# Optimization experiments

Hardware: AMD Instinct MI355X
Metric: run time of the kernel (lower is better)

## Reference

```python
import jax, jax.numpy as jnp
import numpy as np

B, S, D, H = 64, 197, 1024, 4096

# I-BERT IntGELU constants: erf(x) ~ a*(x+b)^2 + c on [0,-b], integer-only form
K_SQRT2 = 1.4142          # sqrt(2)
GELU_SHIFT = 14           # 2**14 right-shift to avoid accumulator overflow
COEF_A = -0.2888
COEF_B = -1.769
COEF_C = 1.0 / COEF_A     # c folded by a, as in I-BERT (coeff[2] /= coeff[0])


def setup_inputs() -> dict:
    key = jax.random.key(0)
    k1, k2, k3, k4, k5, k6 = jax.random.split(key, 6)
    x_int = jax.random.randint(k1, (B, S, D), 0, 127).astype(jnp.int32)  # int8-range activations
    s_x = jax.random.uniform(k2, (1,), jnp.float32, 0.01, 0.03)          # per-tensor act scale
    w1 = jax.random.normal(k3, (H, D), jnp.float32) * 0.02
    b1 = jax.random.normal(k4, (H,), jnp.float32) * 0.02
    w2 = jax.random.normal(k5, (D, H), jnp.float32) * 0.02
    b2 = jax.random.normal(k6, (D,), jnp.float32) * 0.02
    return {"x_int": x_int, "s_x": s_x, "w1": w1, "b1": b1, "w2": w2, "b2": b2}


def _quant_weight(w):
    # per-tensor symmetric int8 weight quantization (QuantLinearWithWeight)
    s_w = jnp.max(jnp.abs(w)) / 127.0
    w_int = jnp.clip(jnp.round(w / s_w), -127.0, 127.0)
    return w_int, s_w


def _quant_linear(x_int, s_x, w, b):
    # integer GEMM: int8 acts x int8 weights -> int32 accumulator, scale s_x*s_w
    w_int, s_w = _quant_weight(w)
    s_out = s_x * s_w
    b_int = jnp.round(b / s_out)  # bias quantized into the accumulator scale
    acc = jnp.einsum('bsd,hd->bsh', x_int, w_int) + b_int
    return acc, s_out


def _int_erf(x_int, sf):
    # integer polynomial approx of erf (I-BERT)
    b_int = jnp.floor(COEF_B / sf)
    c_int = jnp.floor(COEF_C / sf ** 2)
    sign = jnp.sign(x_int)
    abs_int = jnp.minimum(jnp.abs(x_int), -b_int)
    y_int = sign * ((abs_int + b_int) ** 2 + c_int)
    sf_out = sf ** 2 * COEF_A
    y_int = jnp.floor(y_int / 2.0 ** GELU_SHIFT)  # shift to keep accumulator in range
    return y_int, sf_out * 2.0 ** GELU_SHIFT


def _int_gelu(x_int, sf):
    # GELU(x) = x * 0.5 * (1 + erf(x/sqrt(2))), integer-only
    sig_int, sig_sf = _int_erf(x_int, sf / K_SQRT2)
    shift_int = jnp.floor(1.0 / sig_sf)  # torch: 1.0 // sigmoid_scaling_factor
    y_int = x_int * (sig_int + shift_int)
    return y_int, sf * sig_sf / 2.0


def _quant_act(x_int, sf):
    # QuantAct: requantize int32-scale activations back to int8 (dynamic per-tensor scale)
    x_hat = x_int * sf
    s_a = jnp.max(jnp.abs(x_hat)) / 127.0
    q = jnp.clip(jnp.round(x_hat / s_a), -128.0, 127.0)
    return q, s_a


def reference(x_int, s_x, w1, b1, w2, b2):
    x = x_int.astype(jnp.float32)
    s = s_x[0]
    x, s = _quant_linear(x, s, w1, b1)   # [B,S,H] int32 accumulator
    x, s = _int_gelu(x, s)               # integer-only GELU
    x, s = _quant_act(x, s)              # requant -> int8 range
    # dropout_1 is identity in eval mode
    x, s = _quant_linear(x, s, w2, b2)   # [B,S,D] int32 accumulator
    # dropout_2 is identity in eval mode
    return x, s
```

## Files before the change

kernel.cpp:

```cpp
#include <hip/hip_runtime.h>
#include <cstdint>
#include <cstddef>

constexpr int Bb = 64, Ss = 197, Dd = 1024, Hh = 4096;
constexpr int M  = Bb * Ss;
constexpr int MT = (M + 127) / 128;
constexpr int Mpad = MT * 128;
constexpr int NSLOT = 128;

#define SL_MAXW1 0
#define SL_MAXW2 1
#define SL_S1    4
#define SL_BERF  5
#define SL_CERF  6
#define SL_SHIFT 7
#define SL_S2    8
#define SL_SA    9
#define SL_SOUT2 10
#define SL_SW1   11
#define SL_SW2   12
#define SL_MAXY0 16

typedef int v4i __attribute__((ext_vector_type(4)));

#define GLD_LDS(g, l) \
  __builtin_amdgcn_global_load_lds((const __attribute__((address_space(1))) void*)(g), \
                                   (__attribute__((address_space(3))) void*)(l), 16, 0, 0)

__global__ void k_init(unsigned* sl) {
  int t = threadIdx.x;
  if (t < 16 + NSLOT) sl[t] = 0u;
}

__global__ void k_absmax(const float* __restrict__ src, int n4, unsigned* slot) {
  const float4* s4 = (const float4*)src;
  float m = 0.f;
  for (int i = blockIdx.x * blockDim.x + threadIdx.x; i < n4; i += gridDim.x * blockDim.x) {
    float4 v = s4[i];
    m = fmaxf(m, fmaxf(fmaxf(fabsf(v.x), fabsf(v.y)), fmaxf(fabsf(v.z), fabsf(v.w))));
  }
  #pragma unroll
  for (int off = 32; off; off >>= 1) m = fmaxf(m, __shfl_down(m, off, 64));
  __shared__ float wm[4];
  int lane = threadIdx.x & 63, wid = threadIdx.x >> 6;
  if (lane == 0) wm[wid] = m;
  __syncthreads();
  if (threadIdx.x == 0) {
    float b = wm[0];
    for (int i = 1; i < (int)(blockDim.x >> 6); i++) b = fmaxf(b, wm[i]);
    atomicMax(slot, __float_as_uint(b));
  }
}

__global__ void k_scalars1(unsigned* slu, const float* s_x_ptr) {
  float* slf = (float*)slu;
  float s_w1 = __uint_as_float(slu[SL_MAXW1]) / 127.0f;
  float s_w2 = __uint_as_float(slu[SL_MAXW2]) / 127.0f;
  float s1  = s_x_ptr[0] * s_w1;
  float sfe = s1 / 1.4142f;
  float berf = floorf(-1.769f / sfe);
  float cerf = floorf(((float)(1.0 / -0.2888)) / (sfe * sfe));
  float sig  = ((sfe * sfe) * -0.2888f) * 16384.0f;
  float shiftv = floorf(1.0f / sig);
  float s2 = (s1 * sig) / 2.0f;
  slf[SL_S1] = s1; slf[SL_BERF] = berf; slf[SL_CERF] = cerf;
  slf[SL_SHIFT] = shiftv; slf[SL_S2] = s2; slf[SL_SW1] = s_w1; slf[SL_SW2] = s_w2;
}

__global__ void k_scalars2(unsigned* slu, float* dout_scalar) {
  float* slf = (float*)slu;
  float maxy = 0.f;
  for (int i = 0; i < NSLOT; i++) maxy = fmaxf(maxy, __uint_as_float(slu[SL_MAXY0 + i]));
  float xm = fabsf(maxy * slf[SL_S2]);
  float sa = xm / 127.0f;
  float sout2 = sa * slf[SL_SW2];
  slf[SL_SA] = sa; slf[SL_SOUT2] = sout2;
  *dout_scalar = sout2;
}

__global__ void k_quant_w(const float* __restrict__ w, int8_t* __restrict__ wq, int n4,
                          const unsigned* __restrict__ slu, int swslot) {
  float sw = ((const float*)slu)[swslot];
  const float4* w4 = (const float4*)w;
  for (int i = blockIdx.x * blockDim.x + threadIdx.x; i < n4; i += gridDim.x * blockDim.x) {
    float4 v = w4[i];
    int qa = (int)fminf(fmaxf(rintf(v.x / sw), -127.f), 127.f);
    int qb = (int)fminf(fmaxf(rintf(v.y / sw), -127.f), 127.f);
    int qc = (int)fminf(fmaxf(rintf(v.z / sw), -127.f), 127.f);
    int qd = (int)fminf(fmaxf(rintf(v.w / sw), -127.f), 127.f);
    ((unsigned*)wq)[i] = (unsigned)(qa & 0xff) | ((unsigned)(qb & 0xff) << 8) |
                         ((unsigned)(qc & 0xff) << 16) | ((unsigned)(qd & 0xff) << 24);
  }
}

__global__ void k_cvt_x(const int* __restrict__ x, int8_t* __restrict__ xq, int n4, int npad4) {
  const int4* x4 = (const int4*)x;
  for (int i = blockIdx.x * blockDim.x + threadIdx.x; i < npad4; i += gridDim.x * blockDim.x) {
    unsigned p = 0u;
    if (i < n4) {
      int4 v = x4[i];
      p = (unsigned)(v.x & 0xff) | ((unsigned)(v.y & 0xff) << 8) |
          ((unsigned)(v.z & 0xff) << 16) | ((unsigned)(v.w & 0xff) << 24);
    }
    ((unsigned*)xq)[i] = p;
  }
}

template <int K, int MODE, int GN>
__global__ __launch_bounds__(256) void k_gemm(
    const int8_t* __restrict__ A, const int8_t* __restrict__ Bm,
    const float* __restrict__ bias, const unsigned* __restrict__ slu,
    int8_t* __restrict__ qout, float* __restrict__ fout, unsigned* maxslot,
    int Mreal, int Ncols) {
  __shared__ alignas(16) int8_t smem[32768];
  int8_t* As = smem;
  int8_t* Bs = smem + 16384;
  const int t = threadIdx.x;
  const int id = blockIdx.x;
  const int chunk = gridDim.x >> 3;
  const int newid = (id & 7) * chunk + (id >> 3);
  const int bm = newid / GN, bn = newid % GN;
  const int lane = t & 63, wid = t >> 6;
  const int wRow = (wid >> 1) * 64, wCol = (wid & 1) * 64;
  const int lm = lane & 15, quad = lane >> 4;

  v4i acc[4][4] = {};

  const size_t aBase = (size_t)bm * 128 * K;
  const size_t bBase = (size_t)bn * 128 * K;

  for (int k0 = 0; k0 < K; k0 += 128) {
    #pragma unroll
    for (int c = 0; c < 4; c++) {
      int s = c * 256 + t;
      int row = s >> 3;
      int cb = (s & 7) ^ (row & 7);
      size_t goff = (size_t)row * K + k0 + cb * 16;
      GLD_LDS(A + aBase + goff, As + s * 16);
      GLD_LDS(Bm + bBase + goff, Bs + s * 16);
    }
    __syncthreads();
    #pragma unroll
    for (int ks = 0; ks < 2; ks++) {
      v4i af[4], bf[4];
      #pragma unroll
      for (int i = 0; i < 4; i++) {
        int r = wRow + i * 16 + lm;
        af[i] = *(const v4i*)(As + r * 128 + (((ks * 4 + quad) ^ (r & 7)) << 4));
      }
      #pragma unroll
      for (int i = 0; i < 4; i++) {
        int r = wCol + i * 16 + lm;
        bf[i] = *(const v4i*)(Bs + r * 128 + (((ks * 4 + quad) ^ (r & 7)) << 4));
      }
      #pragma unroll
      for (int i = 0; i < 4; i++)
        #pragma unroll
        for (int j = 0; j < 4; j++)
          acc[i][j] = __builtin_amdgcn_mfma_i32_16x16x64_i8(bf[j], af[i], acc[i][j], 0, 0, 0);
    }
    __syncthreads();
  }

  const float* slf = (const float*)slu;
  if constexpr (MODE == 2) {
    float sout2 = slf[SL_SOUT2];
    float4 bq[4];
    #pragma unroll
    for (int j = 0; j < 4; j++) {
      float4 bv = *(const float4*)(bias + bn * 128 + wCol + j * 16 + quad * 4);
      bq[j].x = rintf(bv.x / sout2); bq[j].y = rintf(bv.y / sout2);
      bq[j].z = rintf(bv.z / sout2); bq[j].w = rintf(bv.w / sout2);
    }
    #pragma unroll
    for (int i = 0; i < 4; i++) {
      int gr = bm * 128 + wRow + i * 16 + lm;
      if (gr < Mreal) {
        #pragma unroll
        for (int j = 0; j < 4; j++) {
          int gc0 = bn * 128 + wCol + j * 16 + quad * 4;
          float4 o;
          o.x = (float)acc[i][j][0] + bq[j].x;
          o.y = (float)acc[i][j][1] + bq[j].y;
          o.z = (float)acc[i][j][2] + bq[j].z;
          o.w = (float)acc[i][j][3] + bq[j].w;
          *(float4*)(fout + (size_t)gr * Ncols + gc0) = o;
        }
      }
    }
  } else {
    float s1 = slf[SL_S1], berf = slf[SL_BERF], cerf = slf[SL_CERF], shiftv = slf[SL_SHIFT];
    float s2 = slf[SL_S2];
    float sa = (MODE == 1) ? slf[SL_SA] : 1.0f;
    float r_req = (MODE == 1) ? (s2 / sa) : 1.0f;
    float lmax = 0.f;
    float4 bq[4];
    #pragma unroll
    for (int j = 0; j < 4; j++) {
      float4 bv = *(const float4*)(bias + bn * 128 + wCol + j * 16 + quad * 4);
      bq[j].x = rintf(bv.x / s1); bq[j].y = rintf(bv.y / s1);
      bq[j].z = rintf(bv.z / s1); bq[j].w = rintf(bv.w / s1);
    }
    #pragma unroll
    for (int i = 0; i < 4; i++) {
      int mrow = wRow + i * 16 + lm;
      int gr = bm * 128 + mrow;
      bool rowok = gr < Mreal;
      #pragma unroll
      for (int j = 0; j < 4; j++) {
        int n0 = wCol + j * 16 + quad * 4;
        unsigned packed = 0u;
        #pragma unroll
        for (int r = 0; r < 4; r++) {
          float a = (float)acc[i][j][r] + ((const float*)&bq[j])[r];
          float sgn = (a > 0.f) ? 1.f : ((a < 0.f) ? -1.f : 0.f);
          float ax = fminf(fabsf(a), -berf);
          float tt = ax + berf;
          float yv = sgn * (tt * tt + cerf);
          yv = floorf(yv * (1.0f / 16384.0f));
          float y = a * (yv + shiftv);
          if constexpr (MODE == 0) {
            if (rowok) lmax = fmaxf(lmax, fabsf(y));
          } else {
            float qf = rintf(y * r_req);
            qf = fminf(fmaxf(qf, -128.f), 127.f);
            packed |= ((unsigned)((int)qf & 0xff)) << (8 * r);
          }
        }
        if constexpr (MODE == 1) {
          *(unsigned*)(smem + mrow * 132 + n0) = packed;
        }
      }
    }
    if constexpr (MODE == 0) {
      #pragma unroll
      for (int off = 32; off; off >>= 1) lmax = fmaxf(lmax, __shfl_down(lmax, off, 64));
      float* red = (float*)smem;
      if (lane == 0) red[wid] = lmax;
      __syncthreads();
      if (t == 0) {
        float b = fmaxf(fmaxf(red[0], red[1]), fmaxf(red[2], red[3]));
        atomicMax(maxslot + (id & (NSLOT - 1)), __float_as_uint(b));
      }
    } else {
      __syncthreads();
      #pragma unroll
      for (int c2 = 0; c2 < 4; c2++) {
        int idx = c2 * 256 + t;
        int row = idx >> 3, c16 = (idx & 7) << 4;
        v4i v = *(const v4i*)(smem + row * 132 + c16);
        *(v4i*)(qout + (size_t)(bm * 128 + row) * Ncols + bn * 128 + c16) = v;
      }
    }
  }
}

extern "C" void kernel_launch(void* const* d_in, const int* in_sizes, int n_in,
                              void* d_out, int out_size, void* d_ws, size_t ws_size,
                              hipStream_t stream) {
  const int*   x   = (const int*)d_in[0];
  const float* s_x = (const float*)d_in[1];
  const float* w1  = (const float*)d_in[2];
  const float* b1  = (const float*)d_in[3];
  const float* w2  = (const float*)d_in[4];
  const float* b2  = (const float*)d_in[5];
  float* out = (float*)d_out;

  char* ws = (char*)d_ws;
  unsigned* slots = (unsigned*)ws;
  int8_t* w1q = (int8_t*)(ws + 1024);
  int8_t* w2q = w1q + (size_t)Hh * Dd;
  int8_t* xq  = w2q + (size_t)Dd * Hh;
  int8_t* qbuf = xq + (size_t)Mpad * Dd;

  k_init<<<1, 256, 0, stream>>>(slots);
  k_absmax<<<512, 256, 0, stream>>>(w1, Hh * Dd / 4, slots + SL_MAXW1);
  k_absmax<<<512, 256, 0, stream>>>(w2, Dd * Hh / 4, slots + SL_MAXW2);
  k_scalars1<<<1, 1, 0, stream>>>(slots, s_x);
  k_quant_w<<<512, 256, 0, stream>>>(w1, w1q, Hh * Dd / 4, slots, SL_SW1);
  k_quant_w<<<512, 256, 0, stream>>>(w2, w2q, Dd * Hh / 4, slots, SL_SW2);
  k_cvt_x<<<512, 256, 0, stream>>>(x, xq, M * Dd / 4, Mpad * Dd / 4);

  const int g1 = (Hh / 128) * MT;
  k_gemm<Dd, 0, Hh / 128><<<g1, 256, 0, stream>>>(xq, w1q, b1, slots, nullptr, nullptr,
                                                  slots + SL_MAXY0, M, Hh);
  k_scalars2<<<1, 1, 0, stream>>>(slots, out + (size_t)M * Dd);
  k_gemm<Dd, 1, Hh / 128><<<g1, 256, 0, stream>>>(xq, w1q, b1, slots, qbuf, nullptr,
                                                  nullptr, M, Hh);
  const int g2 = (Dd / 128) * MT;
  k_gemm<Hh, 2, Dd / 128><<<g2, 256, 0, stream>>>(qbuf, w2q, b2, slots, nullptr, out,
                                                  nullptr, M, Dd);
}
```

Before: 428.5 us.

## Enlarge int8 GEMM block tile to 256x128 with one wave per 64-row strip

The int8 MFMA GEMM block tile grows from 128x128 to 256x128. Each wave now owns a 64x128 strip with a 4x8 accumulator array, so it issues more MFMAs per LDS fragment load. LDS grows to 48KB, the launch becomes a 2D grid, and the XCD-aware block-id swizzle is dropped. The change raises arithmetic intensity per byte loaded. In exchange it adds register pressure, lowers occupancy, leaves fewer blocks to fill the CUs, and makes L2 locality depend on default block ordering.

```diff
diff --git a/kernel.cpp b/kernel.cpp
--- a/kernel.cpp
+++ b/kernel.cpp
@@ -4,8 +4,8 @@
 
 constexpr int Bb = 64, Ss = 197, Dd = 1024, Hh = 4096;
 constexpr int M  = Bb * Ss;
-constexpr int MT = (M + 127) / 128;
-constexpr int Mpad = MT * 128;
+constexpr int MT2 = (M + 255) / 256;
+constexpr int Mpad = MT2 * 256;
 constexpr int NSLOT = 128;
 
 #define SL_MAXW1 0
@@ -106,57 +106,59 @@
   }
 }
 
-template <int K, int MODE, int GN>
+template <int K, int MODE>
 __global__ __launch_bounds__(256) void k_gemm(
     const int8_t* __restrict__ A, const int8_t* __restrict__ Bm,
     const float* __restrict__ bias, const unsigned* __restrict__ slu,
     int8_t* __restrict__ qout, float* __restrict__ fout, unsigned* maxslot,
     int Mreal, int Ncols) {
-  __shared__ alignas(16) int8_t smem[32768];
+  __shared__ alignas(16) int8_t smem[49152];
   int8_t* As = smem;
-  int8_t* Bs = smem + 16384;
+  int8_t* Bs = smem + 32768;
   const int t = threadIdx.x;
-  const int id = blockIdx.x;
-  const int chunk = gridDim.x >> 3;
-  const int newid = (id & 7) * chunk + (id >> 3);
-  const int bm = newid / GN, bn = newid % GN;
+  const int bn = blockIdx.x, bm = blockIdx.y;
   const int lane = t & 63, wid = t >> 6;
-  const int wRow = (wid >> 1) * 64, wCol = (wid & 1) * 64;
+  const int wR = wid * 64;
   const int lm = lane & 15, quad = lane >> 4;
 
-  v4i acc[4][4] = {};
-
-  const size_t aBase = (size_t)bm * 128 * K;
+  v4i acc[4][8] = {};
+
+  const size_t aBase = (size_t)bm * 256 * K;
   const size_t bBase = (size_t)bn * 128 * K;
 
   for (int k0 = 0; k0 < K; k0 += 128) {
+    #pragma unroll
+    for (int c = 0; c < 8; c++) {
+      int s = c * 256 + t;
+      int row = s >> 3;
+      int cb = (s & 7) ^ (row & 7);
+      GLD_LDS(A + aBase + (size_t)row * K + k0 + cb * 16, As + s * 16);
+    }
     #pragma unroll
     for (int c = 0; c < 4; c++) {
       int s = c * 256 + t;
       int row = s >> 3;
       int cb = (s & 7) ^ (row & 7);
-      size_t goff = (size_t)row * K + k0 + cb * 16;
-      GLD_LDS(A + aBase + goff, As + s * 16);
-      GLD_LDS(Bm + bBase + goff, Bs + s * 16);
+      GLD_LDS(Bm + bBase + (size_t)row * K + k0 + cb * 16, Bs + s * 16);
     }
     __syncthreads();
     #pragma unroll
     for (int ks = 0; ks < 2; ks++) {
-      v4i af[4], bf[4];
+      v4i af[4], bf[8];
       #pragma unroll
       for (int i = 0; i < 4; i++) {
-        int r = wRow + i * 16 + lm;
+        int r = wR + i * 16 + lm;
         af[i] = *(const v4i*)(As + r * 128 + (((ks * 4 + quad) ^ (r & 7)) << 4));
       }
       #pragma unroll
-      for (int i = 0; i < 4; i++) {
-        int r = wCol + i * 16 + lm;
-        bf[i] = *(const v4i*)(Bs + r * 128 + (((ks * 4 + quad) ^ (r & 7)) << 4));
+      for (int j = 0; j < 8; j++) {
+        int r = j * 16 + lm;
+        bf[j] = *(const v4i*)(Bs + r * 128 + (((ks * 4 + quad) ^ (r & 7)) << 4));
       }
       #pragma unroll
       for (int i = 0; i < 4; i++)
         #pragma unroll
-        for (int j = 0; j < 4; j++)
+        for (int j = 0; j < 8; j++)
           acc[i][j] = __builtin_amdgcn_mfma_i32_16x16x64_i8(bf[j], af[i], acc[i][j], 0, 0, 0);
     }
     __syncthreads();
@@ -165,20 +167,20 @@
   const float* slf = (const float*)slu;
   if constexpr (MODE == 2) {
     float sout2 = slf[SL_SOUT2];
-    float4 bq[4];
-    #pragma unroll
-    for (int j = 0; j < 4; j++) {
-      float4 bv = *(const float4*)(bias + bn * 128 + wCol + j * 16 + quad * 4);
+    float4 bq[8];
+    #pragma unroll
+    for (int j = 0; j < 8; j++) {
+      float4 bv = *(const float4*)(bias + bn * 128 + j * 16 + quad * 4);
       bq[j].x = rintf(bv.x / sout2); bq[j].y = rintf(bv.y / sout2);
       bq[j].z = rintf(bv.z / sout2); bq[j].w = rintf(bv.w / sout2);
     }
     #pragma unroll
     for (int i = 0; i < 4; i++) {
-      int gr = bm * 128 + wRow + i * 16 + lm;
+      int gr = bm * 256 + wR + i * 16 + lm;
       if (gr < Mreal) {
         #pragma unroll
-        for (int j = 0; j < 4; j++) {
-          int gc0 = bn * 128 + wCol + j * 16 + quad * 4;
+        for (int j = 0; j < 8; j++) {
+          int gc0 = bn * 128 + j * 16 + quad * 4;
           float4 o;
           o.x = (float)acc[i][j][0] + bq[j].x;
           o.y = (float)acc[i][j][1] + bq[j].y;
@@ -194,21 +196,21 @@
     float sa = (MODE == 1) ? slf[SL_SA] : 1.0f;
     float r_req = (MODE == 1) ? (s2 / sa) : 1.0f;
     float lmax = 0.f;
-    float4 bq[4];
-    #pragma unroll
-    for (int j = 0; j < 4; j++) {
-      float4 bv = *(const float4*)(bias + bn * 128 + wCol + j * 16 + quad * 4);
+    float4 bq[8];
+    #pragma unroll
+    for (int j = 0; j < 8; j++) {
+      float4 bv = *(const float4*)(bias + bn * 128 + j * 16 + quad * 4);
       bq[j].x = rintf(bv.x / s1); bq[j].y = rintf(bv.y / s1);
       bq[j].z = rintf(bv.z / s1); bq[j].w = rintf(bv.w / s1);
     }
     #pragma unroll
     for (int i = 0; i < 4; i++) {
-      int mrow = wRow + i * 16 + lm;
-      int gr = bm * 128 + mrow;
+      int mrow = wR + i * 16 + lm;
+      int gr = bm * 256 + mrow;
       bool rowok = gr < Mreal;
       #pragma unroll
-      for (int j = 0; j < 4; j++) {
-        int n0 = wCol + j * 16 + quad * 4;
+      for (int j = 0; j < 8; j++) {
+        int n0 = j * 16 + quad * 4;
         unsigned packed = 0u;
         #pragma unroll
         for (int r = 0; r < 4; r++) {
@@ -240,16 +242,17 @@
       __syncthreads();
       if (t == 0) {
         float b = fmaxf(fmaxf(red[0], red[1]), fmaxf(red[2], red[3]));
+        int id = blockIdx.y * gridDim.x + blockIdx.x;
         atomicMax(maxslot + (id & (NSLOT - 1)), __float_as_uint(b));
       }
     } else {
       __syncthreads();
       #pragma unroll
-      for (int c2 = 0; c2 < 4; c2++) {
+      for (int c2 = 0; c2 < 8; c2++) {
         int idx = c2 * 256 + t;
         int row = idx >> 3, c16 = (idx & 7) << 4;
         v4i v = *(const v4i*)(smem + row * 132 + c16);
-        *(v4i*)(qout + (size_t)(bm * 128 + row) * Ncols + bn * 128 + c16) = v;
+        *(v4i*)(qout + (size_t)(bm * 256 + row) * Ncols + bn * 128 + c16) = v;
       }
     }
   }
@@ -281,13 +284,13 @@
   k_quant_w<<<512, 256, 0, stream>>>(w2, w2q, Dd * Hh / 4, slots, SL_SW2);
   k_cvt_x<<<512, 256, 0, stream>>>(x, xq, M * Dd / 4, Mpad * Dd / 4);
 
-  const int g1 = (Hh / 128) * MT;
-  k_gemm<Dd, 0, Hh / 128><<<g1, 256, 0, stream>>>(xq, w1q, b1, slots, nullptr, nullptr,
-                                                  slots + SL_MAXY0, M, Hh);
+  dim3 g1(Hh / 128, MT2);
+  k_gemm<Dd, 0><<<g1, 256, 0, stream>>>(xq, w1q, b1, slots, nullptr, nullptr,
+                                        slots + SL_MAXY0, M, Hh);
   k_scalars2<<<1, 1, 0, stream>>>(slots, out + (size_t)M * Dd);
-  k_gemm<Dd, 1, Hh / 128><<<g1, 256, 0, stream>>>(xq, w1q, b1, slots, qbuf, nullptr,
-                                                  nullptr, M, Hh);
-  const int g2 = (Dd / 128) * MT;
-  k_gemm<Hh, 2, Dd / 128><<<g2, 256, 0, stream>>>(qbuf, w2q, b2, slots, nullptr, out,
-                                                  nullptr, M, Dd);
-}
+  k_gemm<Dd, 1><<<g1, 256, 0, stream>>>(xq, w1q, b1, slots, qbuf, nullptr,
+                                        nullptr, M, Hh);
+  dim3 g2(Dd / 128, MT2);
+  k_gemm<Hh, 2><<<g2, 256, 0, stream>>>(qbuf, w2q, b2, slots, nullptr, out,
+                                        nullptr, M, Dd);
+}
```

Measured after the change: 583.3 us. 1.36x slower.

## Fuse prologue kernels and replace atomic max slots with per-block partials

Applied to the files above, without the earlier changes.

Merges the two weight absmax kernels into one launch and the weight-quantize and activation-convert kernels into one launch. Drops the init kernel by writing per-block partial maxima to workspace arrays and reducing them in parallel scalar kernels, instead of using atomicMax slots. Replaces the XCD-aware block swizzle in the GEMMs with a plain 2D grid, and simplifies the sign handling in the GELU epilogue. Fewer launches and no atomics, at the risk of losing the L2 locality the swizzle provided.

```diff
diff --git a/kernel.cpp b/kernel.cpp
--- a/kernel.cpp
+++ b/kernel.cpp
@@ -6,10 +6,8 @@
 constexpr int M  = Bb * Ss;
 constexpr int MT = (M + 127) / 128;
 constexpr int Mpad = MT * 128;
-constexpr int NSLOT = 128;
-
-#define SL_MAXW1 0
-#define SL_MAXW2 1
+constexpr int NBLK1 = (Hh / 128) * MT;
+
 #define SL_S1    4
 #define SL_BERF  5
 #define SL_CERF  6
@@ -19,7 +17,6 @@
 #define SL_SOUT2 10
 #define SL_SW1   11
 #define SL_SW2   12
-#define SL_MAXY0 16
 
 typedef int v4i __attribute__((ext_vector_type(4)));
 
@@ -27,99 +24,125 @@
   __builtin_amdgcn_global_load_lds((const __attribute__((address_space(1))) void*)(g), \
                                    (__attribute__((address_space(3))) void*)(l), 16, 0, 0)
 
-__global__ void k_init(unsigned* sl) {
-  int t = threadIdx.x;
-  if (t < 16 + NSLOT) sl[t] = 0u;
-}
-
-__global__ void k_absmax(const float* __restrict__ src, int n4, unsigned* slot) {
-  const float4* s4 = (const float4*)src;
-  float m = 0.f;
-  for (int i = blockIdx.x * blockDim.x + threadIdx.x; i < n4; i += gridDim.x * blockDim.x) {
-    float4 v = s4[i];
-    m = fmaxf(m, fmaxf(fmaxf(fabsf(v.x), fabsf(v.y)), fmaxf(fabsf(v.z), fabsf(v.w))));
-  }
+__device__ __forceinline__ float blockmax256(float m) {
   #pragma unroll
   for (int off = 32; off; off >>= 1) m = fmaxf(m, __shfl_down(m, off, 64));
   __shared__ float wm[4];
   int lane = threadIdx.x & 63, wid = threadIdx.x >> 6;
   if (lane == 0) wm[wid] = m;
   __syncthreads();
-  if (threadIdx.x == 0) {
-    float b = wm[0];
-    for (int i = 1; i < (int)(blockDim.x >> 6); i++) b = fmaxf(b, wm[i]);
-    atomicMax(slot, __float_as_uint(b));
-  }
-}
-
-__global__ void k_scalars1(unsigned* slu, const float* s_x_ptr) {
-  float* slf = (float*)slu;
-  float s_w1 = __uint_as_float(slu[SL_MAXW1]) / 127.0f;
-  float s_w2 = __uint_as_float(slu[SL_MAXW2]) / 127.0f;
-  float s1  = s_x_ptr[0] * s_w1;
-  float sfe = s1 / 1.4142f;
-  float berf = floorf(-1.769f / sfe);
-  float cerf = floorf(((float)(1.0 / -0.2888)) / (sfe * sfe));
-  float sig  = ((sfe * sfe) * -0.2888f) * 16384.0f;
-  float shiftv = floorf(1.0f / sig);
-  float s2 = (s1 * sig) / 2.0f;
-  slf[SL_S1] = s1; slf[SL_BERF] = berf; slf[SL_CERF] = cerf;
-  slf[SL_SHIFT] = shiftv; slf[SL_S2] = s2; slf[SL_SW1] = s_w1; slf[SL_SW2] = s_w2;
-}
-
-__global__ void k_scalars2(unsigned* slu, float* dout_scalar) {
-  float* slf = (float*)slu;
-  float maxy = 0.f;
-  for (int i = 0; i < NSLOT; i++) maxy = fmaxf(maxy, __uint_as_float(slu[SL_MAXY0 + i]));
-  float xm = fabsf(maxy * slf[SL_S2]);
-  float sa = xm / 127.0f;
-  float sout2 = sa * slf[SL_SW2];
-  slf[SL_SA] = sa; slf[SL_SOUT2] = sout2;
-  *dout_scalar = sout2;
-}
-
-__global__ void k_quant_w(const float* __restrict__ w, int8_t* __restrict__ wq, int n4,
-                          const unsigned* __restrict__ slu, int swslot) {
-  float sw = ((const float*)slu)[swslot];
-  const float4* w4 = (const float4*)w;
-  for (int i = blockIdx.x * blockDim.x + threadIdx.x; i < n4; i += gridDim.x * blockDim.x) {
-    float4 v = w4[i];
-    int qa = (int)fminf(fmaxf(rintf(v.x / sw), -127.f), 127.f);
-    int qb = (int)fminf(fmaxf(rintf(v.y / sw), -127.f), 127.f);
-    int qc = (int)fminf(fmaxf(rintf(v.z / sw), -127.f), 127.f);
-    int qd = (int)fminf(fmaxf(rintf(v.w / sw), -127.f), 127.f);
-    ((unsigned*)wq)[i] = (unsigned)(qa & 0xff) | ((unsigned)(qb & 0xff) << 8) |
-                         ((unsigned)(qc & 0xff) << 16) | ((unsigned)(qd & 0xff) << 24);
-  }
-}
-
-__global__ void k_cvt_x(const int* __restrict__ x, int8_t* __restrict__ xq, int n4, int npad4) {
-  const int4* x4 = (const int4*)x;
-  for (int i = blockIdx.x * blockDim.x + threadIdx.x; i < npad4; i += gridDim.x * blockDim.x) {
-    unsigned p = 0u;
-    if (i < n4) {
-      int4 v = x4[i];
-      p = (unsigned)(v.x & 0xff) | ((unsigned)(v.y & 0xff) << 8) |
-          ((unsigned)(v.z & 0xff) << 16) | ((unsigned)(v.w & 0xff) << 24);
-    }
-    ((unsigned*)xq)[i] = p;
-  }
-}
-
-template <int K, int MODE, int GN>
+  return fmaxf(fmaxf(wm[0], wm[1]), fmaxf(wm[2], wm[3]));
+}
+
+__global__ void k_wmax(const float* __restrict__ w1, const float* __restrict__ w2,
+                       int n4, float* __restrict__ pmax) {
+  int b = blockIdx.x;
+  const float4* s4 = (const float4*)(b < 512 ? w1 : w2);
+  float m = 0.f;
+  for (int i = (b & 511) * 256 + threadIdx.x; i < n4; i += 512 * 256) {
+    float4 v = s4[i];
+    m = fmaxf(m, fmaxf(fmaxf(fabsf(v.x), fabsf(v.y)), fmaxf(fabsf(v.z), fabsf(v.w))));
+  }
+  m = blockmax256(m);
+  if (threadIdx.x == 0) pmax[b] = m;
+}
+
+__global__ void k_scalars1(unsigned* slu, const float* __restrict__ pmax,
+                           const float* __restrict__ s_x_ptr) {
+  int t = threadIdx.x;
+  float m1 = fmaxf(pmax[t], pmax[t + 256]);
+  float m2 = fmaxf(pmax[512 + t], pmax[768 + t]);
+  __shared__ float r1[256], r2[256];
+  r1[t] = m1; r2[t] = m2;
+  __syncthreads();
+  for (int s = 128; s; s >>= 1) {
+    if (t < s) { r1[t] = fmaxf(r1[t], r1[t + s]); r2[t] = fmaxf(r2[t], r2[t + s]); }
+    __syncthreads();
+  }
+  if (t == 0) {
+    float* slf = (float*)slu;
+    float s_w1 = r1[0] / 127.0f;
+    float s_w2 = r2[0] / 127.0f;
+    float s1  = s_x_ptr[0] * s_w1;
+    float sfe = s1 / 1.4142f;
+    float berf = floorf(-1.769f / sfe);
+    float cerf = floorf(((float)(1.0 / -0.2888)) / (sfe * sfe));
+    float sig  = ((sfe * sfe) * -0.2888f) * 16384.0f;
+    float shiftv = floorf(1.0f / sig);
+    float s2 = (s1 * sig) / 2.0f;
+    slf[SL_S1] = s1; slf[SL_BERF] = berf; slf[SL_CERF] = cerf;
+    slf[SL_SHIFT] = shiftv; slf[SL_S2] = s2; slf[SL_SW1] = s_w1; slf[SL_SW2] = s_w2;
+  }
+}
+
+__global__ void k_scalars2(unsigned* slu, const float* __restrict__ pmax,
+                           float* dout_scalar) {
+  int t = threadIdx.x;
+  float m = 0.f;
+  for (int i = t; i < NBLK1; i += 256) m = fmaxf(m, pmax[i]);
+  __shared__ float r1[256];
+  r1[t] = m;
+  __syncthreads();
+  for (int s = 128; s; s >>= 1) {
+    if (t < s) r1[t] = fmaxf(r1[t], r1[t + s]);
+    __syncthreads();
+  }
+  if (t == 0) {
+    float* slf = (float*)slu;
+    float xm = fabsf(r1[0] * slf[SL_S2]);
+    float sa = xm / 127.0f;
+    float sout2 = sa * slf[SL_SW2];
+    slf[SL_SA] = sa; slf[SL_SOUT2] = sout2;
+    *dout_scalar = sout2;
+  }
+}
+
+__global__ void k_quantcvt(const float* __restrict__ w1, const float* __restrict__ w2,
+                           const int* __restrict__ x, const unsigned* __restrict__ slu,
+                           int8_t* __restrict__ w1q, int8_t* __restrict__ w2q,
+                           int8_t* __restrict__ xq) {
+  const float* slf = (const float*)slu;
+  float sw1 = slf[SL_SW1], sw2 = slf[SL_SW2];
+  const int n1 = Hh * Dd / 4, n2 = Dd * Hh / 4;
+  const int nx = M * Dd / 4, n3 = Mpad * Dd / 4;
+  const int total = n1 + n2 + n3;
+  for (int i = blockIdx.x * blockDim.x + threadIdx.x; i < total; i += gridDim.x * blockDim.x) {
+    if (i < n1 + n2) {
+      bool first = i < n1;
+      int idx = first ? i : i - n1;
+      float sw = first ? sw1 : sw2;
+      float4 v = ((const float4*)(first ? w1 : w2))[idx];
+      int qa = (int)fminf(fmaxf(rintf(v.x / sw), -127.f), 127.f);
+      int qb = (int)fminf(fmaxf(rintf(v.y / sw), -127.f), 127.f);
+      int qc = (int)fminf(fmaxf(rintf(v.z / sw), -127.f), 127.f);
+      int qd = (int)fminf(fmaxf(rintf(v.w / sw), -127.f), 127.f);
+      unsigned p = (unsigned)(qa & 0xff) | ((unsigned)(qb & 0xff) << 8) |
+                   ((unsigned)(qc & 0xff) << 16) | ((unsigned)(qd & 0xff) << 24);
+      ((unsigned*)(first ? w1q : w2q))[idx] = p;
+    } else {
+      int idx = i - n1 - n2;
+      unsigned p = 0u;
+      if (idx < nx) {
+        int4 v = ((const int4*)x)[idx];
+        p = (unsigned)(v.x & 0xff) | ((unsigned)(v.y & 0xff) << 8) |
+            ((unsigned)(v.z & 0xff) << 16) | ((unsigned)(v.w & 0xff) << 24);
+      }
+      ((unsigned*)xq)[idx] = p;
+    }
+  }
+}
+
+template <int K, int MODE>
 __global__ __launch_bounds__(256) void k_gemm(
     const int8_t* __restrict__ A, const int8_t* __restrict__ Bm,
     const float* __restrict__ bias, const unsigned* __restrict__ slu,
-    int8_t* __restrict__ qout, float* __restrict__ fout, unsigned* maxslot,
+    int8_t* __restrict__ qout, float* __restrict__ fout, float* __restrict__ pmax_y,
     int Mreal, int Ncols) {
   __shared__ alignas(16) int8_t smem[32768];
   int8_t* As = smem;
   int8_t* Bs = smem + 16384;
   const int t = threadIdx.x;
-  const int id = blockIdx.x;
-  const int chunk = gridDim.x >> 3;
-  const int newid = (id & 7) * chunk + (id >> 3);
-  const int bm = newid / GN, bn = newid % GN;
+  const int bm = blockIdx.y, bn = blockIdx.x;
   const int lane = t & 63, wid = t >> 6;
   const int wRow = (wid >> 1) * 64, wCol = (wid & 1) * 64;
   const int lm = lane & 15, quad = lane >> 4;
@@ -213,11 +236,11 @@
         #pragma unroll
         for (int r = 0; r < 4; r++) {
           float a = (float)acc[i][j][r] + ((const float*)&bq[j])[r];
-          float sgn = (a > 0.f) ? 1.f : ((a < 0.f) ? -1.f : 0.f);
           float ax = fminf(fabsf(a), -berf);
           float tt = ax + berf;
-          float yv = sgn * (tt * tt + cerf);
-          yv = floorf(yv * (1.0f / 16384.0f));
+          float u = tt * tt + cerf;
+          float ye = (a < 0.f) ? -u : u;
+          float yv = floorf(ye * (1.0f / 16384.0f));
           float y = a * (yv + shiftv);
           if constexpr (MODE == 0) {
             if (rowok) lmax = fmaxf(lmax, fabsf(y));
@@ -240,7 +263,7 @@
       __syncthreads();
       if (t == 0) {
         float b = fmaxf(fmaxf(red[0], red[1]), fmaxf(red[2], red[3]));
-        atomicMax(maxslot + (id & (NSLOT - 1)), __float_as_uint(b));
+        pmax_y[bm * gridDim.x + bn] = b;
       }
     } else {
       __syncthreads();
@@ -268,26 +291,24 @@
 
   char* ws = (char*)d_ws;
   unsigned* slots = (unsigned*)ws;
-  int8_t* w1q = (int8_t*)(ws + 1024);
+  float* pmax_w = (float*)(ws + 1024);
+  float* pmax_y = (float*)(ws + 8192);
+  int8_t* w1q = (int8_t*)(ws + 32768);
   int8_t* w2q = w1q + (size_t)Hh * Dd;
   int8_t* xq  = w2q + (size_t)Dd * Hh;
   int8_t* qbuf = xq + (size_t)Mpad * Dd;
 
-  k_init<<<1, 256, 0, stream>>>(slots);
-  k_absmax<<<512, 256, 0, stream>>>(w1, Hh * Dd / 4, slots + SL_MAXW1);
-  k_absmax<<<512, 256, 0, stream>>>(w2, Dd * Hh / 4, slots + SL_MAXW2);
-  k_scalars1<<<1, 1, 0, stream>>>(slots, s_x);
-  k_quant_w<<<512, 256, 0, stream>>>(w1, w1q, Hh * Dd / 4, slots, SL_SW1);
-  k_quant_w<<<512, 256, 0, stream>>>(w2, w2q, Dd * Hh / 4, slots, SL_SW2);
-  k_cvt_x<<<512, 256, 0, stream>>>(x, xq, M * Dd / 4, Mpad * Dd / 4);
-
-  const int g1 = (Hh / 128) * MT;
-  k_gemm<Dd, 0, Hh / 128><<<g1, 256, 0, stream>>>(xq, w1q, b1, slots, nullptr, nullptr,
-                                                  slots + SL_MAXY0, M, Hh);
-  k_scalars2<<<1, 1, 0, stream>>>(slots, out + (size_t)M * Dd);
-  k_gemm<Dd, 1, Hh / 128><<<g1, 256, 0, stream>>>(xq, w1q, b1, slots, qbuf, nullptr,
-                                                  nullptr, M, Hh);
-  const int g2 = (Dd / 128) * MT;
-  k_gemm<Hh, 2, Dd / 128><<<g2, 256, 0, stream>>>(qbuf, w2q, b2, slots, nullptr, out,
-                                                  nullptr, M, Dd);
-}
+  k_wmax<<<1024, 256, 0, stream>>>(w1, w2, Hh * Dd / 4, pmax_w);
+  k_scalars1<<<1, 256, 0, stream>>>(slots, pmax_w, s_x);
+  k_quantcvt<<<1024, 256, 0, stream>>>(w1, w2, x, slots, w1q, w2q, xq);
+
+  dim3 g1(Hh / 128, MT);
+  k_gemm<Dd, 0><<<g1, 256, 0, stream>>>(xq, w1q, b1, slots, nullptr, nullptr,
+                                        pmax_y, M, Hh);
+  k_scalars2<<<1, 256, 0, stream>>>(slots, pmax_y, out + (size_t)M * Dd);
+  k_gemm<Dd, 1><<<g1, 256, 0, stream>>>(xq, w1q, b1, slots, qbuf, nullptr,
+                                        nullptr, M, Hh);
+  dim3 g2(Dd / 128, MT);
+  k_gemm<Hh, 2><<<g2, 256, 0, stream>>>(qbuf, w2q, b2, slots, nullptr, out,
+                                        nullptr, M, Dd);
+}
```

New measurement: 370.3 us. -13.6%, faster.
